# Kernel optimization log

Hardware: AMD Instinct MI355X
Metric: run time of the kernel (lower is better)

Reference implementation:

```python
import jax, jax.numpy as jnp
import numpy as np

N, D, H, OUT, B = 100000, 512, 1024, 250, 256
EPS = 1e-5


def layernorm(x, g, b):
    m = jnp.mean(x, axis=-1, keepdims=True)
    v = jnp.mean(jnp.square(x - m), axis=-1, keepdims=True)
    return (x - m) * jax.lax.rsqrt(v + EPS) * g + b


def setup_inputs() -> dict:
    key = jax.random.key(0)
    ks = jax.random.split(key, 10)
    s = lambda fan: (2.0 / fan) ** 0.5  # kaiming-ish scale
    return {
        "x": jax.random.normal(ks[0], (N, D), jnp.float32),
        "batch_ids": jnp.sort(jax.random.randint(ks[1], (N,), 0, B)),
        "gW1": jax.random.normal(ks[2], (2 * D, D), jnp.float32) * s(D),
        "gb1": jnp.zeros((2 * D,), jnp.float32),
        "gln_g": jnp.ones((2 * D,), jnp.float32),
        "gln_b": jnp.zeros((2 * D,), jnp.float32),
        "gW2": jax.random.normal(ks[3], (1, 2 * D), jnp.float32) * s(2 * D),
        "gb2": jnp.zeros((1,), jnp.float32),
        "pn_g": jnp.ones((D,), jnp.float32),
        "pn_b": jnp.zeros((D,), jnp.float32),
        "mW1": jax.random.normal(ks[4], (H, D), jnp.float32) * s(D),
        "mb1": jnp.zeros((H,), jnp.float32),
        "mln_g": jnp.ones((H,), jnp.float32),
        "mln_b": jnp.zeros((H,), jnp.float32),
        "mW2": jax.random.normal(ks[5], (OUT, H), jnp.float32) * s(H),
        "mb2": jnp.zeros((OUT,), jnp.float32),
    }


def reference(x, batch_ids, gW1, gb1, gln_g, gln_b, gW2, gb2,
              pn_g, pn_b, mW1, mb1, mln_g, mln_b, mW2, mb2):
    # gate MLP: Linear -> LayerNorm -> ReLU -> Linear(->1)
    h = jax.nn.relu(layernorm(x @ gW1.T + gb1, gln_g, gln_b))  # [N, 2D]
    gate = (h @ gW2.T + gb2)[:, 0]                              # [N]
    # segment-wise softmax over batch_ids
    seg_max = jax.ops.segment_max(gate, batch_ids, num_segments=B)
    e = jnp.exp(gate - jax.lax.stop_gradient(seg_max)[batch_ids])
    denom = jax.ops.segment_sum(e, batch_ids, num_segments=B)
    w = e / denom[batch_ids]                                    # [N]
    pooled = jax.ops.segment_sum(w[:, None] * x, batch_ids, num_segments=B)  # [B, D]
    out = layernorm(pooled, pn_g, pn_b)
    # classifier MLP (dropout = identity in eval)
    z = jax.nn.relu(layernorm(out @ mW1.T + mb1, mln_g, mln_b))
    logits = z @ mW2.T + mb2                                    # [B, OUT]
    return logits
```

## Files before the change

### kernel.cpp

```cpp
#include <hip/hip_runtime.h>
#include <stdint.h>

typedef unsigned int u32;
typedef unsigned short u16;

#define NROWS 100000
#define DIM 512
#define HDIM 1024
#define OUTF 250
#define NSEG 256
#define LNEPS 1e-5f
#define BM 32
#define NG 3125

typedef __bf16 bf16_t;
typedef bf16_t bf16x8 __attribute__((ext_vector_type(8)));
typedef float f32x4 __attribute__((ext_vector_type(4)));

__device__ inline u16 f2bf(float f) {
    u32 u = __float_as_uint(f);
    u = (u + 0x7FFFu + ((u >> 16) & 1u)) >> 16;
    return (u16)u;
}
__device__ inline u32 pack2(float a, float b) {
    return (u32)f2bf(a) | ((u32)f2bf(b) << 16);
}

__device__ inline int lower_bound(const int* __restrict__ a, int n, int v) {
    int lo = 0, hi = n;
    while (lo < hi) {
        int m = (lo + hi) >> 1;
        if (a[m] < v) lo = m + 1; else hi = m;
    }
    return lo;
}

__global__ __launch_bounds__(256) void k_wconv(const float* __restrict__ gW1,
                                               u16* __restrict__ Wf) {
    int gid  = blockIdx.x * 256 + threadIdx.x;
    int lane = gid & 63;
    int grp  = gid >> 6;
    int ks   = grp >> 6, nt = grp & 63;
    int n    = nt * 16 + (lane & 15);
    int k0   = ks * 32 + ((lane >> 4) << 3);
    const float* src = gW1 + (size_t)n * DIM + k0;
    float4 f0 = *reinterpret_cast<const float4*>(src);
    float4 f1 = *reinterpret_cast<const float4*>(src + 4);
    uint4 val;
    val.x = pack2(f0.x, f0.y); val.y = pack2(f0.z, f0.w);
    val.z = pack2(f1.x, f1.y); val.w = pack2(f1.z, f1.w);
    reinterpret_cast<uint4*>(Wf)[gid] = val;
}

__global__ __launch_bounds__(512) void k_gate(
    const float* __restrict__ x, const u16* __restrict__ Wf,
    const float* __restrict__ gb1,
    const float* __restrict__ gln_g, const float* __restrict__ gln_b,
    const float* __restrict__ gW2, const float* __restrict__ gb2,
    float* __restrict__ gate)
{
    __shared__ __align__(16) u16 xlds[BM * DIM];
    __shared__ float redS[8][BM];
    __shared__ float redQ[8][BM];
    __shared__ float meanA[BM], rstdA[BM];

    const int tid  = threadIdx.x;
    const int lane = tid & 63;
    const int w    = tid >> 6;
    const int l15  = lane & 15;
    const int g4   = lane >> 4;
    const int row0 = blockIdx.x * BM;

    #pragma unroll
    for (int uu = 0; uu < 4; ++uu) {
        int lu  = uu * 512 + tid;
        int r   = lu >> 6;
        int u   = lu & 63;
        const float* src = x + (size_t)(row0 + r) * DIM + (u << 3);
        float4 f0 = *reinterpret_cast<const float4*>(src);
        float4 f1 = *reinterpret_cast<const float4*>(src + 4);
        bf16x8 v;
        v[0] = (bf16_t)f0.x; v[1] = (bf16_t)f0.y;
        v[2] = (bf16_t)f0.z; v[3] = (bf16_t)f0.w;
        v[4] = (bf16_t)f1.x; v[5] = (bf16_t)f1.y;
        v[6] = (bf16_t)f1.z; v[7] = (bf16_t)f1.w;
        int phys = r * DIM + ((u ^ (r & 7)) << 3);
        *reinterpret_cast<bf16x8*>(&xlds[phys]) = v;
    }
    __syncthreads();

    f32x4 acc[2][8];
    #pragma unroll
    for (int m = 0; m < 2; ++m)
        #pragma unroll
        for (int t = 0; t < 8; ++t)
            acc[m][t] = (f32x4){0.f, 0.f, 0.f, 0.f};

    const bf16x8* __restrict__ WfB = reinterpret_cast<const bf16x8*>(Wf);

    auto loadB = [&](bf16x8 (&b)[8], int ks) {
        #pragma unroll
        for (int t = 0; t < 8; ++t)
            b[t] = WfB[(ks * 64 + w * 8 + t) * 64 + lane];
    };
    auto loadA = [&](bf16x8 (&a)[2], int ks) {
        #pragma unroll
        for (int m = 0; m < 2; ++m) {
            int r = m * 16 + l15;
            int u = ks * 4 + g4;
            a[m] = *reinterpret_cast<const bf16x8*>(&xlds[r * DIM + ((u ^ (r & 7)) << 3)]);
        }
    };
    auto domfma = [&](bf16x8 (&a)[2], bf16x8 (&b)[8]) {
        #pragma unroll
        for (int m = 0; m < 2; ++m)
            #pragma unroll
            for (int t = 0; t < 8; ++t)
                acc[m][t] = __builtin_amdgcn_mfma_f32_16x16x32_bf16(a[m], b[t], acc[m][t], 0, 0, 0);
    };

    bf16x8 b0[8], b1[8], a0[2], a1[2];
    loadB(b0, 0); loadA(a0, 0);
    #pragma unroll
    for (int ks2 = 0; ks2 < 8; ++ks2) {
        loadB(b1, 2 * ks2 + 1);
        loadA(a1, 2 * ks2 + 1);
        domfma(a0, b0);
        if (ks2 < 7) {
            loadB(b0, 2 * ks2 + 2);
            loadA(a0, 2 * ks2 + 2);
        }
        domfma(a1, b1);
    }

    float cbias[8];
    #pragma unroll
    for (int t = 0; t < 8; ++t) cbias[t] = gb1[(w * 8 + t) * 16 + l15];
    #pragma unroll
    for (int m = 0; m < 2; ++m)
        #pragma unroll
        for (int t = 0; t < 8; ++t)
            #pragma unroll
            for (int j = 0; j < 4; ++j)
                acc[m][t][j] += cbias[t];

    #pragma unroll
    for (int m = 0; m < 2; ++m) {
        #pragma unroll
        for (int j = 0; j < 4; ++j) {
            float s1 = 0.f, s2 = 0.f;
            #pragma unroll
            for (int t = 0; t < 8; ++t) {
                float v = acc[m][t][j];
                s1 += v; s2 += v * v;
            }
            #pragma unroll
            for (int off = 1; off < 16; off <<= 1) {
                s1 += __shfl_xor(s1, off);
                s2 += __shfl_xor(s2, off);
            }
            if (l15 == 0) {
                int row = m * 16 + g4 * 4 + j;
                redS[w][row] = s1;
                redQ[w][row] = s2;
            }
        }
    }
    __syncthreads();
    if (tid < BM) {
        float S1 = 0.f, S2 = 0.f;
        #pragma unroll
        for (int ww = 0; ww < 8; ++ww) { S1 += redS[ww][tid]; S2 += redQ[ww][tid]; }
        float mean = S1 * (1.0f / 1024.0f);
        float var  = S2 * (1.0f / 1024.0f) - mean * mean;
        meanA[tid] = mean;
        rstdA[tid] = rsqrtf(var + LNEPS);
    }
    __syncthreads();

    float cg[8], cb[8], cw[8];
    #pragma unroll
    for (int t = 0; t < 8; ++t) {
        int c = (w * 8 + t) * 16 + l15;
        cg[t] = gln_g[c]; cb[t] = gln_b[c]; cw[t] = gW2[c];
    }
    #pragma unroll
    for (int m = 0; m < 2; ++m) {
        #pragma unroll
        for (int j = 0; j < 4; ++j) {
            int row = m * 16 + g4 * 4 + j;
            float mn = meanA[row];
            float rs = rstdA[row];
            float gp = 0.f;
            #pragma unroll
            for (int t = 0; t < 8; ++t) {
                float h = (acc[m][t][j] - mn) * rs * cg[t] + cb[t];
                gp += fmaxf(h, 0.f) * cw[t];
            }
            #pragma unroll
            for (int off = 1; off < 16; off <<= 1)
                gp += __shfl_xor(gp, off);
            if (l15 == 0) redS[w][row] = gp;
        }
    }
    __syncthreads();
    if (tid < BM) {
        float s = gb2[0];
        #pragma unroll
        for (int ww = 0; ww < 8; ++ww) s += redS[ww][tid];
        gate[row0 + tid] = s;
    }
}

__global__ __launch_bounds__(256) void k_seg(const int* __restrict__ ids,
                                             const float* __restrict__ gate,
                                             float* __restrict__ segmax,
                                             float* __restrict__ segden) {
    int b = blockIdx.x, tid = threadIdx.x;
    int start = lower_bound(ids, NROWS, b);
    int end   = lower_bound(ids, NROWS, b + 1);
    __shared__ float sh[4];

    float lm = -INFINITY;
    for (int i = start + tid; i < end; i += 256) lm = fmaxf(lm, gate[i]);
    #pragma unroll
    for (int off = 32; off; off >>= 1) lm = fmaxf(lm, __shfl_xor(lm, off));
    if ((tid & 63) == 0) sh[tid >> 6] = lm;
    __syncthreads();
    float m = fmaxf(fmaxf(sh[0], sh[1]), fmaxf(sh[2], sh[3]));
    __syncthreads();

    float ls = 0.f;
    for (int i = start + tid; i < end; i += 256) ls += __expf(gate[i] - m);
    #pragma unroll
    for (int off = 32; off; off >>= 1) ls += __shfl_xor(ls, off);
    if ((tid & 63) == 0) sh[tid >> 6] = ls;
    __syncthreads();
    if (tid == 0) {
        segmax[b] = m;
        segden[b] = sh[0] + sh[1] + sh[2] + sh[3];
    }
}

__global__ __launch_bounds__(512) void k_pool(const int* __restrict__ ids,
                                              const float* __restrict__ gate,
                                              const float* __restrict__ x,
                                              const float* __restrict__ segmax,
                                              const float* __restrict__ segden,
                                              float* __restrict__ pooled) {
    const int b = blockIdx.x, tid = threadIdx.x;
    const int slot   = tid & 127;
    const int stripe = tid >> 7;
    const int start = lower_bound(ids, NROWS, b);
    const int end   = lower_bound(ids, NROWS, b + 1);
    const float m   = segmax[b];
    const float den = segden[b];
    const float inv = (den > 0.f) ? 1.0f / den : 0.0f;

    __shared__ f32x4 sh[4][128];

    const f32x4* __restrict__ xr = reinterpret_cast<const f32x4*>(x);
    f32x4 acc = (f32x4){0.f, 0.f, 0.f, 0.f};
    for (int i = start + stripe; i < end; i += 4) {
        float wgt = __expf(gate[i] - m) * inv;
        f32x4 xv = xr[(size_t)i * 128 + slot];
        acc += wgt * xv;
    }
    sh[stripe][slot] = acc;
    __syncthreads();
    if (tid < 128) {
        f32x4 r = sh[0][tid] + sh[1][tid] + sh[2][tid] + sh[3][tid];
        reinterpret_cast<f32x4*>(pooled)[b * 128 + tid] = r;
    }
}

__device__ inline float block_sum(float v, float* sh, int tid) {
    #pragma unroll
    for (int off = 32; off; off >>= 1) v += __shfl_xor(v, off);
    if ((tid & 63) == 0) sh[tid >> 6] = v;
    __syncthreads();
    float r = sh[0] + sh[1] + sh[2] + sh[3];
    __syncthreads();
    return r;
}

__global__ __launch_bounds__(256) void k_head(
    const float* __restrict__ pooled,
    const float* __restrict__ pn_g, const float* __restrict__ pn_b,
    const float* __restrict__ mW1, const float* __restrict__ mb1,
    const float* __restrict__ mln_g, const float* __restrict__ mln_b,
    const float* __restrict__ mW2, const float* __restrict__ mb2,
    float* __restrict__ logits)
{
    const int b = blockIdx.x, tid = threadIdx.x;
    __shared__ float outr[DIM];
    __shared__ float zr[HDIM];
    __shared__ float shred[4];

    float v0 = pooled[b * DIM + tid];
    float v1 = pooled[b * DIM + 256 + tid];
    float S = block_sum(v0 + v1, shred, tid);
    float Q = block_sum(v0 * v0 + v1 * v1, shred, tid);
    float mean = S * (1.0f / 512.0f);
    float rstd = rsqrtf(Q * (1.0f / 512.0f) - mean * mean + LNEPS);
    outr[tid]       = (v0 - mean) * rstd * pn_g[tid] + pn_b[tid];
    outr[tid + 256] = (v1 - mean) * rstd * pn_g[tid + 256] + pn_b[tid + 256];
    __syncthreads();

    float y[4];
    #pragma unroll
    for (int q = 0; q < 4; ++q) {
        int f = q * 256 + tid;
        const float4* wr = reinterpret_cast<const float4*>(mW1 + (size_t)f * DIM);
        float acc = 0.f;
        #pragma unroll 8
        for (int kk = 0; kk < 128; ++kk) {
            float4 wv = wr[kk];
            acc += wv.x * outr[kk * 4 + 0] + wv.y * outr[kk * 4 + 1]
                 + wv.z * outr[kk * 4 + 2] + wv.w * outr[kk * 4 + 3];
        }
        y[q] = acc + mb1[f];
    }
    float S2 = block_sum(y[0] + y[1] + y[2] + y[3], shred, tid);
    float Q2 = block_sum(y[0]*y[0] + y[1]*y[1] + y[2]*y[2] + y[3]*y[3], shred, tid);
    float mean2 = S2 * (1.0f / 1024.0f);
    float rstd2 = rsqrtf(Q2 * (1.0f / 1024.0f) - mean2 * mean2 + LNEPS);
    #pragma unroll
    for (int q = 0; q < 4; ++q) {
        int f = q * 256 + tid;
        zr[f] = fmaxf((y[q] - mean2) * rstd2 * mln_g[f] + mln_b[f], 0.f);
    }
    __syncthreads();
    if (tid < OUTF) {
        const float4* wr = reinterpret_cast<const float4*>(mW2 + (size_t)tid * HDIM);
        float acc = 0.f;
        #pragma unroll 8
        for (int kk = 0; kk < 256; ++kk) {
            float4 wv = wr[kk];
            acc += wv.x * zr[kk * 4 + 0] + wv.y * zr[kk * 4 + 1]
                 + wv.z * zr[kk * 4 + 2] + wv.w * zr[kk * 4 + 3];
        }
        logits[b * OUTF + tid] = acc + mb2[tid];
    }
}

extern "C" void kernel_launch(void* const* d_in, const int* in_sizes, int n_in,
                              void* d_out, int out_size, void* d_ws, size_t ws_size,
                              hipStream_t stream) {
    const float* x     = (const float*)d_in[0];
    const int*   ids   = (const int*)  d_in[1];
    const float* gW1   = (const float*)d_in[2];
    const float* gb1   = (const float*)d_in[3];
    const float* gln_g = (const float*)d_in[4];
    const float* gln_b = (const float*)d_in[5];
    const float* gW2   = (const float*)d_in[6];
    const float* gb2   = (const float*)d_in[7];
    const float* pn_g  = (const float*)d_in[8];
    const float* pn_b  = (const float*)d_in[9];
    const float* mW1   = (const float*)d_in[10];
    const float* mb1   = (const float*)d_in[11];
    const float* mln_g = (const float*)d_in[12];
    const float* mln_b = (const float*)d_in[13];
    const float* mW2   = (const float*)d_in[14];
    const float* mb2   = (const float*)d_in[15];
    float* logits = (float*)d_out;

    char* ws = (char*)d_ws;
    u16*   Wf     = (u16*)  (ws);
    float* gate   = (float*)(ws + (1 << 20));
    float* segmax = (float*)(ws + (1 << 20) + 409600);
    float* segden = segmax + 256;
    float* pooled = (float*)(ws + (1 << 20) + 409600 + 4096);

    hipLaunchKernelGGL(k_wconv, dim3(256), dim3(256), 0, stream, gW1, Wf);
    hipLaunchKernelGGL(k_gate, dim3(NG), dim3(512), 0, stream,
                       x, Wf, gb1, gln_g, gln_b, gW2, gb2, gate);
    hipLaunchKernelGGL(k_seg, dim3(NSEG), dim3(256), 0, stream, ids, gate, segmax, segden);
    hipLaunchKernelGGL(k_pool, dim3(NSEG), dim3(512), 0, stream,
                       ids, gate, x, segmax, segden, pooled);
    hipLaunchKernelGGL(k_head, dim3(NSEG), dim3(256), 0, stream,
                       pooled, pn_g, pn_b, mW1, mb1, mln_g, mln_b, mW2, mb2, logits);
}
```

Baseline: 302.4 us.

## Split pooling four ways and run classifier head as batched bf16 MFMA GEMMs

```diff
diff --git a/kernel.cpp b/kernel.cpp
--- a/kernel.cpp
+++ b/kernel.cpp
@@ -14,17 +14,9 @@
 #define NG 3125
 
 typedef __bf16 bf16_t;
+typedef bf16_t bf16x4 __attribute__((ext_vector_type(4)));
 typedef bf16_t bf16x8 __attribute__((ext_vector_type(8)));
 typedef float f32x4 __attribute__((ext_vector_type(4)));
-
-__device__ inline u16 f2bf(float f) {
-    u32 u = __float_as_uint(f);
-    u = (u + 0x7FFFu + ((u >> 16) & 1u)) >> 16;
-    return (u16)u;
-}
-__device__ inline u32 pack2(float a, float b) {
-    return (u32)f2bf(a) | ((u32)f2bf(b) << 16);
-}
 
 __device__ inline int lower_bound(const int* __restrict__ a, int n, int v) {
     int lo = 0, hi = n;
@@ -35,21 +27,53 @@
     return lo;
 }
 
-__global__ __launch_bounds__(256) void k_wconv(const float* __restrict__ gW1,
-                                               u16* __restrict__ Wf) {
-    int gid  = blockIdx.x * 256 + threadIdx.x;
-    int lane = gid & 63;
-    int grp  = gid >> 6;
-    int ks   = grp >> 6, nt = grp & 63;
-    int n    = nt * 16 + (lane & 15);
-    int k0   = ks * 32 + ((lane >> 4) << 3);
-    const float* src = gW1 + (size_t)n * DIM + k0;
-    float4 f0 = *reinterpret_cast<const float4*>(src);
-    float4 f1 = *reinterpret_cast<const float4*>(src + 4);
-    uint4 val;
-    val.x = pack2(f0.x, f0.y); val.y = pack2(f0.z, f0.w);
-    val.z = pack2(f1.x, f1.y); val.w = pack2(f1.z, f1.w);
-    reinterpret_cast<uint4*>(Wf)[gid] = val;
+__global__ __launch_bounds__(256) void k_conv(const float* __restrict__ gW1,
+                                              const float* __restrict__ mW1,
+                                              const float* __restrict__ mW2,
+                                              u16* __restrict__ Wf,
+                                              u16* __restrict__ mW1f,
+                                              u16* __restrict__ mW2f) {
+    int bid = blockIdx.x;
+    if (bid < 512) {
+        const float* src_base = (bid < 256) ? gW1 : mW1;
+        u16* dst = (bid < 256) ? Wf : mW1f;
+        int gid  = (bid & 255) * 256 + threadIdx.x;
+        int lane = gid & 63;
+        int grp  = gid >> 6;
+        int ks   = grp >> 6, nt = grp & 63;
+        int n    = nt * 16 + (lane & 15);
+        int k0   = ks * 32 + ((lane >> 4) << 3);
+        const float* src = src_base + (size_t)n * DIM + k0;
+        float4 f0 = *reinterpret_cast<const float4*>(src);
+        float4 f1 = *reinterpret_cast<const float4*>(src + 4);
+        bf16x8 v;
+        v[0] = (bf16_t)f0.x; v[1] = (bf16_t)f0.y;
+        v[2] = (bf16_t)f0.z; v[3] = (bf16_t)f0.w;
+        v[4] = (bf16_t)f1.x; v[5] = (bf16_t)f1.y;
+        v[6] = (bf16_t)f1.z; v[7] = (bf16_t)f1.w;
+        reinterpret_cast<bf16x8*>(dst)[gid] = v;
+    } else {
+        int gid  = (bid - 512) * 256 + threadIdx.x;
+        int lane = gid & 63;
+        int grp  = gid >> 6;
+        int ks   = grp >> 4, nt = grp & 15;
+        int n    = nt * 16 + (lane & 15);
+        int k0   = ks * 32 + ((lane >> 4) << 3);
+        bf16x8 v;
+        if (n < OUTF) {
+            const float* src = mW2 + (size_t)n * HDIM + k0;
+            float4 f0 = *reinterpret_cast<const float4*>(src);
+            float4 f1 = *reinterpret_cast<const float4*>(src + 4);
+            v[0] = (bf16_t)f0.x; v[1] = (bf16_t)f0.y;
+            v[2] = (bf16_t)f0.z; v[3] = (bf16_t)f0.w;
+            v[4] = (bf16_t)f1.x; v[5] = (bf16_t)f1.y;
+            v[6] = (bf16_t)f1.z; v[7] = (bf16_t)f1.w;
+        } else {
+            #pragma unroll
+            for (int j = 0; j < 8; ++j) v[j] = (bf16_t)0.f;
+        }
+        reinterpret_cast<bf16x8*>(mW2f)[gid] = v;
+    }
 }
 
 __global__ __launch_bounds__(512) void k_gate(
@@ -242,13 +266,13 @@
     }
 }
 
-__global__ __launch_bounds__(512) void k_pool(const int* __restrict__ ids,
-                                              const float* __restrict__ gate,
-                                              const float* __restrict__ x,
-                                              const float* __restrict__ segmax,
-                                              const float* __restrict__ segden,
-                                              float* __restrict__ pooled) {
-    const int b = blockIdx.x, tid = threadIdx.x;
+__global__ __launch_bounds__(512) void k_poolp(const int* __restrict__ ids,
+                                               const float* __restrict__ gate,
+                                               const float* __restrict__ x,
+                                               const float* __restrict__ segmax,
+                                               const float* __restrict__ segden,
+                                               float* __restrict__ pooledp) {
+    const int b = blockIdx.x, q = blockIdx.y, tid = threadIdx.x;
     const int slot   = tid & 127;
     const int stripe = tid >> 7;
     const int start = lower_bound(ids, NROWS, b);
@@ -261,7 +285,7 @@
 
     const f32x4* __restrict__ xr = reinterpret_cast<const f32x4*>(x);
     f32x4 acc = (f32x4){0.f, 0.f, 0.f, 0.f};
-    for (int i = start + stripe; i < end; i += 4) {
+    for (int i = start + q * 4 + stripe; i < end; i += 16) {
         float wgt = __expf(gate[i] - m) * inv;
         f32x4 xv = xr[(size_t)i * 128 + slot];
         acc += wgt * xv;
@@ -270,77 +294,210 @@
     __syncthreads();
     if (tid < 128) {
         f32x4 r = sh[0][tid] + sh[1][tid] + sh[2][tid] + sh[3][tid];
-        reinterpret_cast<f32x4*>(pooled)[b * 128 + tid] = r;
-    }
-}
-
-__device__ inline float block_sum(float v, float* sh, int tid) {
-    #pragma unroll
-    for (int off = 32; off; off >>= 1) v += __shfl_xor(v, off);
-    if ((tid & 63) == 0) sh[tid >> 6] = v;
-    __syncthreads();
-    float r = sh[0] + sh[1] + sh[2] + sh[3];
-    __syncthreads();
-    return r;
-}
-
-__global__ __launch_bounds__(256) void k_head(
-    const float* __restrict__ pooled,
-    const float* __restrict__ pn_g, const float* __restrict__ pn_b,
-    const float* __restrict__ mW1, const float* __restrict__ mb1,
-    const float* __restrict__ mln_g, const float* __restrict__ mln_b,
-    const float* __restrict__ mW2, const float* __restrict__ mb2,
-    float* __restrict__ logits)
-{
+        reinterpret_cast<f32x4*>(pooledp)[(q * NSEG + b) * 128 + tid] = r;
+    }
+}
+
+__global__ __launch_bounds__(128) void k_pln(const float* __restrict__ pooledp,
+                                             const float* __restrict__ pn_g,
+                                             const float* __restrict__ pn_b,
+                                             u16* __restrict__ outbf) {
     const int b = blockIdx.x, tid = threadIdx.x;
-    __shared__ float outr[DIM];
-    __shared__ float zr[HDIM];
-    __shared__ float shred[4];
-
-    float v0 = pooled[b * DIM + tid];
-    float v1 = pooled[b * DIM + 256 + tid];
-    float S = block_sum(v0 + v1, shred, tid);
-    float Q = block_sum(v0 * v0 + v1 * v1, shred, tid);
+    const f32x4* pp = reinterpret_cast<const f32x4*>(pooledp);
+    f32x4 v = pp[(0 * NSEG + b) * 128 + tid] + pp[(1 * NSEG + b) * 128 + tid]
+            + pp[(2 * NSEG + b) * 128 + tid] + pp[(3 * NSEG + b) * 128 + tid];
+    float s = v[0] + v[1] + v[2] + v[3];
+    float q = v[0]*v[0] + v[1]*v[1] + v[2]*v[2] + v[3]*v[3];
+    #pragma unroll
+    for (int off = 32; off; off >>= 1) {
+        s += __shfl_xor(s, off);
+        q += __shfl_xor(q, off);
+    }
+    __shared__ float sh[4];
+    if ((tid & 63) == 0) { sh[(tid >> 6) * 2] = s; sh[(tid >> 6) * 2 + 1] = q; }
+    __syncthreads();
+    float S = sh[0] + sh[2], Q = sh[1] + sh[3];
     float mean = S * (1.0f / 512.0f);
     float rstd = rsqrtf(Q * (1.0f / 512.0f) - mean * mean + LNEPS);
-    outr[tid]       = (v0 - mean) * rstd * pn_g[tid] + pn_b[tid];
-    outr[tid + 256] = (v1 - mean) * rstd * pn_g[tid + 256] + pn_b[tid + 256];
-    __syncthreads();
-
-    float y[4];
-    #pragma unroll
-    for (int q = 0; q < 4; ++q) {
-        int f = q * 256 + tid;
-        const float4* wr = reinterpret_cast<const float4*>(mW1 + (size_t)f * DIM);
-        float acc = 0.f;
-        #pragma unroll 8
-        for (int kk = 0; kk < 128; ++kk) {
-            float4 wv = wr[kk];
-            acc += wv.x * outr[kk * 4 + 0] + wv.y * outr[kk * 4 + 1]
-                 + wv.z * outr[kk * 4 + 2] + wv.w * outr[kk * 4 + 3];
-        }
-        y[q] = acc + mb1[f];
-    }
-    float S2 = block_sum(y[0] + y[1] + y[2] + y[3], shred, tid);
-    float Q2 = block_sum(y[0]*y[0] + y[1]*y[1] + y[2]*y[2] + y[3]*y[3], shred, tid);
-    float mean2 = S2 * (1.0f / 1024.0f);
-    float rstd2 = rsqrtf(Q2 * (1.0f / 1024.0f) - mean2 * mean2 + LNEPS);
-    #pragma unroll
-    for (int q = 0; q < 4; ++q) {
-        int f = q * 256 + tid;
-        zr[f] = fmaxf((y[q] - mean2) * rstd2 * mln_g[f] + mln_b[f], 0.f);
-    }
-    __syncthreads();
-    if (tid < OUTF) {
-        const float4* wr = reinterpret_cast<const float4*>(mW2 + (size_t)tid * HDIM);
-        float acc = 0.f;
-        #pragma unroll 8
-        for (int kk = 0; kk < 256; ++kk) {
-            float4 wv = wr[kk];
-            acc += wv.x * zr[kk * 4 + 0] + wv.y * zr[kk * 4 + 1]
-                 + wv.z * zr[kk * 4 + 2] + wv.w * zr[kk * 4 + 3];
-        }
-        logits[b * OUTF + tid] = acc + mb2[tid];
+    f32x4 g = reinterpret_cast<const f32x4*>(pn_g)[tid];
+    f32x4 bb = reinterpret_cast<const f32x4*>(pn_b)[tid];
+    bf16x4 o;
+    #pragma unroll
+    for (int j = 0; j < 4; ++j)
+        o[j] = (bf16_t)((v[j] - mean) * rstd * g[j] + bb[j]);
+    reinterpret_cast<bf16x4*>(outbf)[b * 128 + tid] = o;
+}
+
+__global__ __launch_bounds__(512) void k_heady(const u16* __restrict__ outbf,
+                                               const u16* __restrict__ mW1f,
+                                               const float* __restrict__ mb1,
+                                               float* __restrict__ y) {
+    __shared__ __align__(16) u16 alds[128 * DIM];
+    const int tid  = threadIdx.x;
+    const int lane = tid & 63;
+    const int w    = tid >> 6;
+    const int wm   = w >> 2;
+    const int wn   = w & 3;
+    const int l15  = lane & 15;
+    const int g4   = lane >> 4;
+    const int hc   = blockIdx.x;
+    const int sh_  = blockIdx.y;
+
+    const uint4* srcU = reinterpret_cast<const uint4*>(outbf);
+    #pragma unroll
+    for (int uu = 0; uu < 16; ++uu) {
+        int lu = uu * 512 + tid;
+        int r  = lu >> 6;
+        int u  = lu & 63;
+        uint4 val = srcU[(size_t)(sh_ * 128 + r) * 64 + u];
+        int phys = r * DIM + ((u ^ (r & 7)) << 3);
+        *reinterpret_cast<uint4*>(&alds[phys]) = val;
+    }
+    __syncthreads();
+
+    f32x4 acc[4][4];
+    #pragma unroll
+    for (int m = 0; m < 4; ++m)
+        #pragma unroll
+        for (int t = 0; t < 4; ++t)
+            acc[m][t] = (f32x4){0.f, 0.f, 0.f, 0.f};
+
+    const bf16x8* __restrict__ WB = reinterpret_cast<const bf16x8*>(mW1f);
+    #pragma unroll 4
+    for (int ks = 0; ks < 16; ++ks) {
+        bf16x8 b[4];
+        #pragma unroll
+        for (int t = 0; t < 4; ++t) {
+            int nt_g = hc * 16 + wn * 4 + t;
+            b[t] = WB[(ks * 64 + nt_g) * 64 + lane];
+        }
+        bf16x8 a[4];
+        #pragma unroll
+        for (int m = 0; m < 4; ++m) {
+            int r = wm * 64 + m * 16 + l15;
+            int u = ks * 4 + g4;
+            a[m] = *reinterpret_cast<const bf16x8*>(&alds[r * DIM + ((u ^ (r & 7)) << 3)]);
+        }
+        #pragma unroll
+        for (int m = 0; m < 4; ++m)
+            #pragma unroll
+            for (int t = 0; t < 4; ++t)
+                acc[m][t] = __builtin_amdgcn_mfma_f32_16x16x32_bf16(a[m], b[t], acc[m][t], 0, 0, 0);
+    }
+
+    #pragma unroll
+    for (int t = 0; t < 4; ++t) {
+        int col = hc * 256 + (wn * 4 + t) * 16 + l15;
+        float bias = mb1[col];
+        #pragma unroll
+        for (int m = 0; m < 4; ++m)
+            #pragma unroll
+            for (int j = 0; j < 4; ++j) {
+                int seg = sh_ * 128 + wm * 64 + m * 16 + g4 * 4 + j;
+                y[(size_t)seg * HDIM + col] = acc[m][t][j] + bias;
+            }
+    }
+}
+
+__global__ __launch_bounds__(256) void k_headz(const float* __restrict__ y,
+                                               const float* __restrict__ mln_g,
+                                               const float* __restrict__ mln_b,
+                                               u16* __restrict__ zbf) {
+    const int b = blockIdx.x, tid = threadIdx.x;
+    f32x4 v = reinterpret_cast<const f32x4*>(y)[b * 256 + tid];
+    float s = v[0] + v[1] + v[2] + v[3];
+    float q = v[0]*v[0] + v[1]*v[1] + v[2]*v[2] + v[3]*v[3];
+    #pragma unroll
+    for (int off = 32; off; off >>= 1) {
+        s += __shfl_xor(s, off);
+        q += __shfl_xor(q, off);
+    }
+    __shared__ float sh[8];
+    if ((tid & 63) == 0) { sh[(tid >> 6) * 2] = s; sh[(tid >> 6) * 2 + 1] = q; }
+    __syncthreads();
+    float S = sh[0] + sh[2] + sh[4] + sh[6];
+    float Q = sh[1] + sh[3] + sh[5] + sh[7];
+    float mean = S * (1.0f / 1024.0f);
+    float rstd = rsqrtf(Q * (1.0f / 1024.0f) - mean * mean + LNEPS);
+    f32x4 g = reinterpret_cast<const f32x4*>(mln_g)[tid];
+    f32x4 bb = reinterpret_cast<const f32x4*>(mln_b)[tid];
+    bf16x4 o;
+    #pragma unroll
+    for (int j = 0; j < 4; ++j)
+        o[j] = (bf16_t)fmaxf((v[j] - mean) * rstd * g[j] + bb[j], 0.f);
+    reinterpret_cast<bf16x4*>(zbf)[b * 256 + tid] = o;
+}
+
+__global__ __launch_bounds__(512) void k_logits(const u16* __restrict__ zbf,
+                                                const u16* __restrict__ mW2f,
+                                                const float* __restrict__ mb2,
+                                                float* __restrict__ logits) {
+    __shared__ __align__(16) u16 alds[128 * 256];
+    const int tid  = threadIdx.x;
+    const int lane = tid & 63;
+    const int w    = tid >> 6;
+    const int wm   = w >> 2;
+    const int wn   = w & 3;
+    const int l15  = lane & 15;
+    const int g4   = lane >> 4;
+    const int sh_  = blockIdx.x;
+
+    f32x4 acc[4][4];
+    #pragma unroll
+    for (int m = 0; m < 4; ++m)
+        #pragma unroll
+        for (int t = 0; t < 4; ++t)
+            acc[m][t] = (f32x4){0.f, 0.f, 0.f, 0.f};
+
+    const uint4* srcU = reinterpret_cast<const uint4*>(zbf);
+    const bf16x8* __restrict__ WB = reinterpret_cast<const bf16x8*>(mW2f);
+
+    for (int kc = 0; kc < 4; ++kc) {
+        __syncthreads();
+        #pragma unroll
+        for (int uu = 0; uu < 8; ++uu) {
+            int lu = uu * 512 + tid;
+            int r  = lu >> 5;
+            int u  = lu & 31;
+            uint4 val = srcU[(size_t)(sh_ * 128 + r) * 128 + kc * 32 + u];
+            int phys = r * 256 + ((u ^ (r & 7)) << 3);
+            *reinterpret_cast<uint4*>(&alds[phys]) = val;
+        }
+        __syncthreads();
+        #pragma unroll
+        for (int ksl = 0; ksl < 8; ++ksl) {
+            bf16x8 b[4];
+            #pragma unroll
+            for (int t = 0; t < 4; ++t)
+                b[t] = WB[((kc * 8 + ksl) * 16 + wn * 4 + t) * 64 + lane];
+            bf16x8 a[4];
+            #pragma unroll
+            for (int m = 0; m < 4; ++m) {
+                int r = wm * 64 + m * 16 + l15;
+                int u = ksl * 4 + g4;
+                a[m] = *reinterpret_cast<const bf16x8*>(&alds[r * 256 + ((u ^ (r & 7)) << 3)]);
+            }
+            #pragma unroll
+            for (int m = 0; m < 4; ++m)
+                #pragma unroll
+                for (int t = 0; t < 4; ++t)
+                    acc[m][t] = __builtin_amdgcn_mfma_f32_16x16x32_bf16(a[m], b[t], acc[m][t], 0, 0, 0);
+        }
+    }
+
+    #pragma unroll
+    for (int t = 0; t < 4; ++t) {
+        int col = (wn * 4 + t) * 16 + l15;
+        if (col < OUTF) {
+            float bias = mb2[col];
+            #pragma unroll
+            for (int m = 0; m < 4; ++m)
+                #pragma unroll
+                for (int j = 0; j < 4; ++j) {
+                    int seg = sh_ * 128 + wm * 64 + m * 16 + g4 * 4 + j;
+                    logits[(size_t)seg * OUTF + col] = acc[m][t][j] + bias;
+                }
+        }
     }
 }
 
@@ -366,18 +523,32 @@
     float* logits = (float*)d_out;
 
     char* ws = (char*)d_ws;
-    u16*   Wf     = (u16*)  (ws);
-    float* gate   = (float*)(ws + (1 << 20));
-    float* segmax = (float*)(ws + (1 << 20) + 409600);
-    float* segden = segmax + 256;
-    float* pooled = (float*)(ws + (1 << 20) + 409600 + 4096);
-
-    hipLaunchKernelGGL(k_wconv, dim3(256), dim3(256), 0, stream, gW1, Wf);
+    const size_t MB = 1 << 20;
+    u16*   Wf      = (u16*)  (ws);
+    u16*   mW1f    = (u16*)  (ws + 1 * MB);
+    u16*   mW2f    = (u16*)  (ws + 2 * MB);
+    float* gate    = (float*)(ws + 5 * MB / 2);
+    float* segmax  = (float*)(ws + 3 * MB);
+    float* segden  = segmax + NSEG;
+    float* pooledp = (float*)(ws + 4 * MB);
+    u16*   outbf   = (u16*)  (ws + 6 * MB);
+    float* y       = (float*)(ws + 7 * MB);
+    u16*   zbf     = (u16*)  (ws + 8 * MB);
+
+    hipLaunchKernelGGL(k_conv, dim3(640), dim3(256), 0, stream,
+                       gW1, mW1, mW2, Wf, mW1f, mW2f);
     hipLaunchKernelGGL(k_gate, dim3(NG), dim3(512), 0, stream,
                        x, Wf, gb1, gln_g, gln_b, gW2, gb2, gate);
-    hipLaunchKernelGGL(k_seg, dim3(NSEG), dim3(256), 0, stream, ids, gate, segmax, segden);
-    hipLaunchKernelGGL(k_pool, dim3(NSEG), dim3(512), 0, stream,
-                       ids, gate, x, segmax, segden, pooled);
-    hipLaunchKernelGGL(k_head, dim3(NSEG), dim3(256), 0, stream,
-                       pooled, pn_g, pn_b, mW1, mb1, mln_g, mln_b, mW2, mb2, logits);
-}
+    hipLaunchKernelGGL(k_seg, dim3(NSEG), dim3(256), 0, stream,
+                       ids, gate, segmax, segden);
+    hipLaunchKernelGGL(k_poolp, dim3(NSEG, 4), dim3(512), 0, stream,
+                       ids, gate, x, segmax, segden, pooledp);
+    hipLaunchKernelGGL(k_pln, dim3(NSEG), dim3(128), 0, stream,
+                       pooledp, pn_g, pn_b, outbf);
+    hipLaunchKernelGGL(k_heady, dim3(4, 2), dim3(512), 0, stream,
+                       outbf, mW1f, mb1, y);
+    hipLaunchKernelGGL(k_headz, dim3(NSEG), dim3(256), 0, stream,
+                       y, mln_g, mln_b, zbf);
+    hipLaunchKernelGGL(k_logits, dim3(2), dim3(512), 0, stream,
+                       zbf, mW2f, mb2, logits);
+}
```

After: 245.7 us. 18.7% less time.
